# Performance work log

Measured on AMD Instinct MI355X. Metric: run time of the kernel, lower is better.

Reference implementation:

```python
import jax, jax.numpy as jnp
import numpy as np
from jax import lax

N = 8192          # river-network nodes
B = 2             # batch
T = 1024          # time steps (hours)
W = 64            # max_delay (IRF support)
H = 256           # MLP hidden dim
DT = 1.0 / 24.0   # dt in days
D_LEVELS = 8      # tree depth (4-ary tree with 8192 nodes -> depths 0..7)
BRANCH = 4


def _tree():
    parent = np.zeros(N, np.int32)
    depth = np.zeros(N, np.int32)
    for i in range(1, N):
        p = (i - 1) // BRANCH
        parent[i] = p
        depth[i] = depth[p] + 1
    parent[0] = N  # root drains to dummy sink (row N is dropped after scatter)
    return parent, depth


def setup_inputs() -> dict:
    key = jax.random.key(0)
    ks = jax.random.split(key, 6)
    parent, depth = _tree()
    return {
        "x": jax.random.uniform(ks[0], (B, N, T), dtype=jnp.float32),
        "phys": jax.random.normal(ks[1], (N, 3), dtype=jnp.float32),
        "w1": jax.random.normal(ks[2], (3, H), dtype=jnp.float32) * 0.3,
        "b1": jnp.zeros((H,), jnp.float32),
        "w2": jax.random.normal(ks[3], (H, H), dtype=jnp.float32) * 0.05,
        "b2": jnp.zeros((H,), jnp.float32),
        "w3": jax.random.normal(ks[4], (H, 2), dtype=jnp.float32) * 0.05,
        "b3": jnp.zeros((2,), jnp.float32),
        "parent": jnp.asarray(parent),
        "depth": jnp.asarray(depth),
    }


def _mlp(phys, w1, b1, w2, b2, w3, b3):
    h = jax.nn.relu(phys @ w1 + b1)
    h = jax.nn.relu(h @ w2 + b2)
    return h @ w3 + b3  # [N, 2]


def _params(phys, w1, b1, w2, b2, w3, b3):
    raw = _mlp(phys, w1, b1, w2, b2, w3, b3)
    pre_sig_off = jnp.array([0.0, 3.0], jnp.float32)
    rng = jnp.array([0.25, 1.2], jnp.float32)
    off = jnp.array([0.005, 0.0], jnp.float32)
    p = jax.nn.sigmoid(raw - pre_sig_off) * rng + off
    return p[:, 0], p[:, 1]  # Muskingum k (days), x (weight)


def _muskingum_irf(k, xw):
    # Linear-channel Muskingum IRF: pure delay k*x then exponential store k*(1-x).
    t = jnp.arange(W, dtype=jnp.float32) * DT            # [W]
    delay = (k * xw)[:, None]                            # [N, 1]
    tau = jnp.maximum(k * (1.0 - xw), 0.5 * DT)[:, None]  # keep store positive
    h = jnp.where(t[None, :] >= delay,
                  jnp.exp(-(t[None, :] - delay) / tau) / tau, 0.0)
    return h / (h.sum(-1, keepdims=True) + 1e-8)          # [N, W], unit mass


def _causal_conv(sig, irf):
    # sig [B, N, T], irf [N, W]; depthwise causal conv along time per node.
    rhs = irf[:, None, ::-1]  # [N, 1, W], reversed so correlation == convolution
    return lax.conv_general_dilated(
        sig, rhs, window_strides=(1,), padding=[(W - 1, 0)],
        dimension_numbers=("NCH", "OIH", "NCH"), feature_group_count=N)


def _route(x, irf, parent, depth):
    # Leaves-to-root routing: out[i] = irf_i * (x[i] + sum_children out[child]).
    out = jnp.zeros_like(x)
    acc = x
    for d in range(D_LEVELS - 1, -1, -1):
        mask = (depth == d)[None, :, None]
        routed = _causal_conv(acc, irf)
        contrib = jnp.where(mask, routed, 0.0)
        out = out + contrib
        upd = jnp.zeros((B, N + 1, T), x.dtype).at[:, parent, :].add(contrib)
        acc = acc + upd[:, :N, :]
    return out


def reference(x, phys, w1, b1, w2, b2, w3, b3, parent, depth):
    k, xw = _params(phys, w1, b1, w2, b2, w3, b3)
    irf = _muskingum_irf(k, xw)
    return _route(x, irf, parent, depth)  # [B, N, T]
```

## Files before the change

### kernel.cpp

```cpp
#include <hip/hip_runtime.h>
#include <hip/hip_bf16.h>

#define NN 8192
#define TT 1024
#define WW 64
#define HH 256
#define DTF (1.0f/24.0f)

typedef __attribute__((ext_vector_type(8))) short short8_t;
typedef __attribute__((ext_vector_type(4))) short short4_t;
typedef __attribute__((ext_vector_type(4))) float f32x4_t;

__device__ __forceinline__ float sigmoidf_(float v) { return 1.0f / (1.0f + __expf(-v)); }

__device__ __forceinline__ short f2bf(float f) {
    __hip_bfloat16 h = __float2bfloat16(f);
    short s; __builtin_memcpy(&s, &h, sizeof(short));
    return s;
}

__device__ __forceinline__ int swz(int e) { return e ^ (((e >> 6) & 3) << 3); }

__global__ __launch_bounds__(256) void mlp_mfma(
    const float* __restrict__ phys,
    const float* __restrict__ w1, const float* __restrict__ b1,
    const float* __restrict__ w2, const float* __restrict__ b2,
    const float* __restrict__ w3, const float* __restrict__ b3,
    float* __restrict__ irf, short* __restrict__ irfB)
{
    const int t    = threadIdx.x;
    const int wv   = t >> 6;
    const int lane = t & 63;
    const int lc = lane & 15, lg = lane >> 4;
    const int n0 = blockIdx.x * 16;

    __shared__ float s_phys[16 * 3];
    __shared__ __align__(16) short s_h1b[16 * 256];
    __shared__ float s_red[4][16][2];
    __shared__ float s_kxw[16][2];
    __shared__ __align__(16) float s_irf[16 * 64];

    if (t < 48) s_phys[t] = phys[n0 * 3 + t];
    __syncthreads();

    {
        const int m  = t >> 4;
        const int i0 = (t & 15) * 16;
        const float p0 = s_phys[m*3+0], p1 = s_phys[m*3+1], p2 = s_phys[m*3+2];
        float h[16];
#pragma unroll
        for (int u = 0; u < 4; ++u) {
            const float4 a0 = *(const float4*)&w1[0*HH + i0 + 4*u];
            const float4 a1 = *(const float4*)&w1[1*HH + i0 + 4*u];
            const float4 a2 = *(const float4*)&w1[2*HH + i0 + 4*u];
            const float4 bb = *(const float4*)&b1[i0 + 4*u];
            h[4*u+0] = fmaxf(p0*a0.x + p1*a1.x + p2*a2.x + bb.x, 0.f);
            h[4*u+1] = fmaxf(p0*a0.y + p1*a1.y + p2*a2.y + bb.y, 0.f);
            h[4*u+2] = fmaxf(p0*a0.z + p1*a1.z + p2*a2.z + bb.z, 0.f);
            h[4*u+3] = fmaxf(p0*a0.w + p1*a1.w + p2*a2.w + bb.w, 0.f);
        }
#pragma unroll
        for (int u = 0; u < 2; ++u) {
            short8_t s;
#pragma unroll
            for (int j = 0; j < 8; ++j) s[j] = f2bf(h[8*u + j]);
            *(short8_t*)&s_h1b[m * 256 + ((i0 + 8*u) ^ ((m & 7) << 3))] = s;
        }
    }
    __syncthreads();

    f32x4_t acc[4];
#pragma unroll
    for (int u = 0; u < 4; ++u) acc[u] = f32x4_t{0.f, 0.f, 0.f, 0.f};
    short8_t af[8];
#pragma unroll
    for (int ks = 0; ks < 8; ++ks)
        af[ks] = *(const short8_t*)&s_h1b[lc * 256 + ((ks*32 + 8*lg) ^ ((lc & 7) << 3))];
#pragma unroll
    for (int u = 0; u < 4; ++u) {
        const int nt = 4 * wv + u;
#pragma unroll
        for (int ks = 0; ks < 8; ++ks) {
            short8_t bfr;
#pragma unroll
            for (int j = 0; j < 8; ++j)
                bfr[j] = f2bf(w2[(ks*32 + 8*lg + j) * HH + nt*16 + lc]);
            acc[u] = __builtin_amdgcn_mfma_f32_16x16x32_bf16(af[ks], bfr, acc[u], 0, 0, 0);
        }
    }

    float p3[4][2];
#pragma unroll
    for (int q = 0; q < 4; ++q) { p3[q][0] = 0.f; p3[q][1] = 0.f; }
#pragma unroll
    for (int u = 0; u < 4; ++u) {
        const int j = (4*wv + u) * 16 + lc;
        const float b2v = b2[j];
        const float w30 = w3[j*2+0], w31 = w3[j*2+1];
#pragma unroll
        for (int q = 0; q < 4; ++q) {
            const float h2 = fmaxf(acc[u][q] + b2v, 0.f);
            p3[q][0] += h2 * w30; p3[q][1] += h2 * w31;
        }
    }
#pragma unroll
    for (int off = 8; off >= 1; off >>= 1)
#pragma unroll
        for (int q = 0; q < 4; ++q) {
            p3[q][0] += __shfl_xor(p3[q][0], off);
            p3[q][1] += __shfl_xor(p3[q][1], off);
        }
    if (lc == 0)
#pragma unroll
        for (int q = 0; q < 4; ++q) {
            s_red[wv][4*lg + q][0] = p3[q][0];
            s_red[wv][4*lg + q][1] = p3[q][1];
        }
    __syncthreads();

    if (t < 32) {
        const int m = t >> 1, d = t & 1;
        const float raw = s_red[0][m][d] + s_red[1][m][d] + s_red[2][m][d] + s_red[3][m][d] + b3[d];
        s_kxw[m][d] = (d == 0) ? sigmoidf_(raw) * 0.25f + 0.005f
                               : sigmoidf_(raw - 3.f) * 1.2f;
    }
    __syncthreads();

    {
        const int nd = t >> 4, l = t & 15;
        const float k = s_kxw[nd][0], xw = s_kxw[nd][1];
        const float delay = k * xw;
        const float tau   = fmaxf(k * (1.f - xw), 0.5f * DTF);
        float hv[4]; float s = 0.f;
#pragma unroll
        for (int u = 0; u < 4; ++u) {
            const float tf = (l + 16*u) * DTF;
            hv[u] = (tf >= delay) ? __expf(-(tf - delay) / tau) / tau : 0.f;
            s += hv[u];
        }
#pragma unroll
        for (int off = 8; off >= 1; off >>= 1) s += __shfl_xor(s, off);
        const float inv = 1.f / (s + 1e-8f);
        float* drow = irf + (size_t)(n0 + nd) * WW;
#pragma unroll
        for (int u = 0; u < 4; ++u) {
            const float v = hv[u] * inv;
            drow[l + 16*u]        = v;
            s_irf[nd*64 + l + 16*u] = v;
        }
    }
    __syncthreads();

    {
        const int nd = t >> 4, lb = t & 15;
        const float* sr = &s_irf[nd * 64];
        short* dst = irfB + (size_t)(n0 + nd) * 1536;
#pragma unroll
        for (int li = 0; li < 4; ++li) {
            const int L = 4*lb + li;
            const int Llc = L & 15, Llg = L >> 4;
#pragma unroll
            for (int p = 0; p < 3; ++p) {
                short8_t v;
#pragma unroll
                for (int j = 0; j < 8; ++j) {
                    const int idx = Llc - 8*Llg - j + 16 + 32*p;
                    v[j] = f2bf((idx >= 0 && idx < 64) ? sr[idx & 63] : 0.f);
                }
                *(short8_t*)&dst[(size_t)(p*64 + L) * 8] = v;
            }
        }
    }
}

#define LROW 1152

__device__ __forceinline__ void zero_prologue(short* sab, int tid) {
    if (tid < 10) {
        short8_t z = {0,0,0,0,0,0,0,0};
        *(short8_t*)&sab[swz(8 * tid)] = z;
    }
}

__device__ __forceinline__ void load16(const float* __restrict__ src, int tid, float (&a)[16]) {
#pragma unroll
    for (int u = 0; u < 4; ++u) {
        const float4 v = *(const float4*)&src[16 * tid + 4 * u];
        a[4*u+0] = v.x; a[4*u+1] = v.y; a[4*u+2] = v.z; a[4*u+3] = v.w;
    }
}

__device__ __forceinline__ void stage16(short* sab, const float (&a)[16], int tid) {
#pragma unroll
    for (int u = 0; u < 2; ++u) {
        short8_t s;
#pragma unroll
        for (int j = 0; j < 8; ++j) s[j] = f2bf(a[8*u + j]);
        *(short8_t*)&sab[swz(80 + 16 * tid + 8 * u)] = s;
    }
}

__device__ __forceinline__ void load_bfrags(const short* __restrict__ irfB, int n,
                                            int tid, short8_t (&bf)[3]) {
#pragma unroll
    for (int p = 0; p < 3; ++p)
        bf[p] = *(const short8_t*)&irfB[(size_t)n * 1536 + (size_t)(p*64 + tid) * 8];
}

__device__ __forceinline__ void conv_mfma3(const short* sab, const short8_t (&bf)[3],
                                           int EB, f32x4_t (&acc)[4]) {
#pragma unroll
    for (int S = 0; S < 4; ++S) {
#pragma unroll
        for (int p = 0; p < 3; ++p) {
            const short8_t af = *(const short8_t*)&sab[swz(EB + 256 * S - 16 * (2 * p + 1))];
            acc[S] = __builtin_amdgcn_mfma_f32_16x16x32_bf16(bf[p], af, acc[S], 0, 0, 0);
        }
    }
}

__global__ __launch_bounds__(256) void route_lf6p(
    const float* __restrict__ x, const short* __restrict__ irfB,
    float* __restrict__ out)
{
    const int wid = threadIdx.x >> 6;
    const int tid = threadIdx.x & 63;
    const int r   = blockIdx.x * 4 + wid;
    if (r >= 3074) return;

    const int lc = tid & 15, lg = tid >> 4;
    const int EB = 80 + 16 * lc + 8 * lg;
    const int DP = 16 * lc + 4 * lg;

    __shared__ __align__(16) short s_a[4][LROW];
    short* sab = s_a[wid];
    zero_prologue(sab, tid);

    float a16[16];
    short8_t bf[3];

    if (r < 3072) {
        const bool isl6 = (r < 1366);
        const int idx = isl6 ? r : (r - 1366);
        const int b = idx & 1;
        const int n = __builtin_amdgcn_readfirstlane((isl6 ? 1365 : 512) + (idx >> 1));
        const size_t rowb = ((size_t)b * NN + n) * TT;
        const int c0 = 4 * n + 1;

        f32x4_t accD[4];
#pragma unroll
        for (int S = 0; S < 4; ++S)
            accD[S] = *(const f32x4_t*)&x[rowb + 256 * S + DP];

#pragma unroll 1
        for (int e = 0; e < 4; ++e) {
            const int c = c0 + e;
            if (c < NN) {
                const size_t crow = ((size_t)b * NN + c) * TT;
                load16(x + crow, tid, a16);
                stage16(sab, a16, tid);
                load_bfrags(irfB, c, tid, bf);
                f32x4_t accT[4];
#pragma unroll
                for (int S = 0; S < 4; ++S) accT[S] = f32x4_t{0.f, 0.f, 0.f, 0.f};
                conv_mfma3(sab, bf, EB, accT);
#pragma unroll
                for (int S = 0; S < 4; ++S) {
                    *(f32x4_t*)&out[crow + 256 * S + DP] = accT[S];
                    accD[S] += accT[S];
                }
            }
        }

#pragma unroll
        for (int S = 0; S < 4; ++S) {
            short4_t s4;
#pragma unroll
            for (int q = 0; q < 4; ++q) s4[q] = f2bf(accD[S][q]);
            *(short4_t*)&sab[swz(80 + 256 * S + DP)] = s4;
        }

        load_bfrags(irfB, n, tid, bf);
        f32x4_t accF[4];
#pragma unroll
        for (int S = 0; S < 4; ++S) accF[S] = f32x4_t{0.f, 0.f, 0.f, 0.f};
        conv_mfma3(sab, bf, EB, accF);
#pragma unroll
        for (int S = 0; S < 4; ++S)
            *(f32x4_t*)&out[rowb + 256 * S + DP] = accF[S];
    } else {
        const int b = r - 3072;
        const int n = 2048;
        const size_t rowb = ((size_t)b * NN + n) * TT;

        load16(x + rowb, tid, a16);
        stage16(sab, a16, tid);
        load_bfrags(irfB, n, tid, bf);
        f32x4_t accF[4];
#pragma unroll
        for (int S = 0; S < 4; ++S) accF[S] = f32x4_t{0.f, 0.f, 0.f, 0.f};
        conv_mfma3(sab, bf, EB, accF);
#pragma unroll
        for (int S = 0; S < 4; ++S)
            *(f32x4_t*)&out[rowb + 256 * S + DP] = accF[S];
    }
}

__global__ __launch_bounds__(256) void route_mid_mfma(
    const float* __restrict__ x, const short* __restrict__ irfB,
    float* __restrict__ out, int base, int n_tasks)
{
    const int wid = threadIdx.x >> 6;
    const int tid = threadIdx.x & 63;
    const int r   = blockIdx.x * 4 + wid;
    if (r >= n_tasks) return;

    const int lc = tid & 15, lg = tid >> 4;
    const int EB = 80 + 16 * lc + 8 * lg;
    const int DP = 16 * lc + 4 * lg;

    __shared__ __align__(16) short s_a[4][LROW];
    short* sab = s_a[wid];
    zero_prologue(sab, tid);

    const int b = r & 1;
    const int n = __builtin_amdgcn_readfirstlane(base + (r >> 1));
    const size_t rowb = ((size_t)b * NN + n) * TT;
    const int c0 = 4 * n + 1;

    float a16[16];
#pragma unroll
    for (int u = 0; u < 4; ++u) {
        float4 v = *(const float4*)&x[rowb + 16 * tid + 4 * u];
#pragma unroll
        for (int e = 0; e < 4; ++e) {
            const float4 w = *(const float4*)&out[((size_t)b * NN + c0 + e) * TT + 16 * tid + 4 * u];
            v.x += w.x; v.y += w.y; v.z += w.z; v.w += w.w;
        }
        a16[4*u+0] = v.x; a16[4*u+1] = v.y; a16[4*u+2] = v.z; a16[4*u+3] = v.w;
    }
    stage16(sab, a16, tid);

    short8_t bf[3];
    load_bfrags(irfB, n, tid, bf);
    f32x4_t accF[4];
#pragma unroll
    for (int S = 0; S < 4; ++S) accF[S] = f32x4_t{0.f, 0.f, 0.f, 0.f};
    conv_mfma3(sab, bf, EB, accF);
#pragma unroll
    for (int S = 0; S < 4; ++S)
        *(f32x4_t*)&out[rowb + 256 * S + DP] = accF[S];
}

__global__ __launch_bounds__(256) void route_tail3_mfma(
    const float* __restrict__ x, const short* __restrict__ irfB,
    float* __restrict__ out)
{
    const int wid = threadIdx.x >> 6;
    const int tid = threadIdx.x & 63;
    const int b   = blockIdx.x & 1;
    const int p   = 5 + (int)(blockIdx.x >> 1);

    const int lc = tid & 15, lg = tid >> 4;
    const int EB = 80 + 16 * lc + 8 * lg;
    const int DP = 16 * lc + 4 * lg;

    __shared__ __align__(16) short s_a[4][LROW];
    __shared__ __align__(16) float s_ch[4][TT];
    short* sab = s_a[wid];
    zero_prologue(sab, tid);

    const int cw = 4 * p + 1 + wid;
    const size_t crow = ((size_t)b * NN + cw) * TT;

    float a16[16];
    short8_t bf[3];

    f32x4_t accCW[4];
#pragma unroll
    for (int S = 0; S < 4; ++S)
        accCW[S] = *(const f32x4_t*)&x[crow + 256 * S + DP];

#pragma unroll 1
    for (int k = 0; k < 4; ++k) {
        const int g = 4 * cw + 1 + k;
        const size_t grow = ((size_t)b * NN + g) * TT;
#pragma unroll
        for (int u = 0; u < 4; ++u) {
            float4 v = *(const float4*)&x[grow + 16 * tid + 4 * u];
#pragma unroll
            for (int e = 0; e < 4; ++e) {
                const float4 w = *(const float4*)&out[((size_t)b * NN + (4 * g + 1 + e)) * TT + 16 * tid + 4 * u];
                v.x += w.x; v.y += w.y; v.z += w.z; v.w += w.w;
            }
            a16[4*u+0] = v.x; a16[4*u+1] = v.y; a16[4*u+2] = v.z; a16[4*u+3] = v.w;
        }
        stage16(sab, a16, tid);
        load_bfrags(irfB, g, tid, bf);
        f32x4_t accT[4];
#pragma unroll
        for (int S = 0; S < 4; ++S) accT[S] = f32x4_t{0.f, 0.f, 0.f, 0.f};
        conv_mfma3(sab, bf, EB, accT);
#pragma unroll
        for (int S = 0; S < 4; ++S) {
            *(f32x4_t*)&out[grow + 256 * S + DP] = accT[S];
            accCW[S] += accT[S];
        }
    }

#pragma unroll
    for (int S = 0; S < 4; ++S) {
        short4_t s4;
#pragma unroll
        for (int q = 0; q < 4; ++q) s4[q] = f2bf(accCW[S][q]);
        *(short4_t*)&sab[swz(80 + 256 * S + DP)] = s4;
    }
    load_bfrags(irfB, cw, tid, bf);
    f32x4_t accB[4];
#pragma unroll
    for (int S = 0; S < 4; ++S) accB[S] = f32x4_t{0.f, 0.f, 0.f, 0.f};
    conv_mfma3(sab, bf, EB, accB);
#pragma unroll
    for (int S = 0; S < 4; ++S) {
        *(f32x4_t*)&out[crow + 256 * S + DP] = accB[S];
        *(f32x4_t*)&s_ch[wid][256 * S + DP]  = accB[S];
    }

    __syncthreads();

    if (wid == 0) {
        const size_t prow = ((size_t)b * NN + p) * TT;
#pragma unroll
        for (int u = 0; u < 4; ++u) {
            float4 v = *(const float4*)&x[prow + 16 * tid + 4 * u];
#pragma unroll
            for (int w2 = 0; w2 < 4; ++w2) {
                const float4 cc = *(const float4*)&s_ch[w2][16 * tid + 4 * u];
                v.x += cc.x; v.y += cc.y; v.z += cc.z; v.w += cc.w;
            }
            a16[4*u+0] = v.x; a16[4*u+1] = v.y; a16[4*u+2] = v.z; a16[4*u+3] = v.w;
        }
        stage16(sab, a16, tid);
        load_bfrags(irfB, p, tid, bf);
        f32x4_t accF[4];
#pragma unroll
        for (int S = 0; S < 4; ++S) accF[S] = f32x4_t{0.f, 0.f, 0.f, 0.f};
        conv_mfma3(sab, bf, EB, accF);
#pragma unroll
        for (int S = 0; S < 4; ++S)
            *(f32x4_t*)&out[prow + 256 * S + DP] = accF[S];
    }
}

__device__ __forceinline__ void load_rf(const float* __restrict__ irf, int n, float (&rf)[WW]) {
    const float* irp = irf + (size_t)n * WW;
#pragma unroll
    for (int i = 0; i < WW / 4; ++i) {
        const float4 f = *(const float4*)&irp[4 * i];
        rf[4*i+0] = f.x; rf[4*i+1] = f.y; rf[4*i+2] = f.z; rf[4*i+3] = f.w;
    }
}

__device__ __forceinline__ void wave_conv16(const float (&a)[16], const float (&rf)[WW],
                                            float (&y)[16], int tid)
{
#pragma unroll
    for (int j = 0; j < 16; ++j) y[j] = 0.0f;
#pragma unroll
    for (int m = 0; m < 16; ++m)
#pragma unroll
        for (int j = m; j < 16; ++j)
            y[j] += rf[j - m] * a[m];
#pragma unroll
    for (int d = 1; d <= 4; ++d) {
        float h[16];
#pragma unroll
        for (int m = 0; m < 16; ++m) {
            const float ha = __shfl(a[m], tid - d);
            h[m] = (tid >= d) ? ha : 0.0f;
        }
        if (d < 4) {
#pragma unroll
            for (int m = 0; m < 16; ++m)
#pragma unroll
                for (int j = 0; j < 16; ++j)
                    y[j] += rf[j + 16 * d - m] * h[m];
        } else {
#pragma unroll
            for (int m = 1; m < 16; ++m)
#pragma unroll
                for (int j = 0; j < m; ++j)
                    y[j] += rf[j + WW - m] * h[m];
        }
    }
}

__global__ __launch_bounds__(256) void route_tail2(
    const float* __restrict__ x, const float* __restrict__ irf,
    float* __restrict__ out)
{
    const int wid = threadIdx.x >> 6;
    const int tid = threadIdx.x & 63;
    const int b   = blockIdx.x;

    __shared__ __align__(16) float s_ch[4][TT];

    const int cw = 1 + wid;
    const size_t crow = ((size_t)b * NN + cw) * TT;
    const int loc = tid * 16;

    float rf[WW], a[16], y[16];

#pragma unroll
    for (int u = 0; u < 4; ++u) {
        float4 v = *(const float4*)&x[crow + loc + 4 * u];
#pragma unroll
        for (int e = 0; e < 4; ++e) {
            const float4 w = *(const float4*)&out[((size_t)b * NN + (4 * cw + 1 + e)) * TT + loc + 4 * u];
            v.x += w.x; v.y += w.y; v.z += w.z; v.w += w.w;
        }
        a[4*u+0] = v.x; a[4*u+1] = v.y; a[4*u+2] = v.z; a[4*u+3] = v.w;
    }
    load_rf(irf, cw, rf);
    wave_conv16(a, rf, y, tid);
#pragma unroll
    for (int u = 0; u < 4; ++u) {
        const float4 f = make_float4(y[4*u+0], y[4*u+1], y[4*u+2], y[4*u+3]);
        *(float4*)&out[crow + loc + 4 * u] = f;
        *(float4*)&s_ch[wid][loc + 4 * u]  = f;
    }

    __syncthreads();

    if (wid == 0) {
        const size_t prow = (size_t)b * NN * TT;
#pragma unroll
        for (int u = 0; u < 4; ++u) {
            float4 v = *(const float4*)&x[prow + loc + 4 * u];
#pragma unroll
            for (int w2 = 0; w2 < 4; ++w2) {
                const float4 cc = *(const float4*)&s_ch[w2][loc + 4 * u];
                v.x += cc.x; v.y += cc.y; v.z += cc.z; v.w += cc.w;
            }
            a[4*u+0] = v.x; a[4*u+1] = v.y; a[4*u+2] = v.z; a[4*u+3] = v.w;
        }
        load_rf(irf, 0, rf);
        wave_conv16(a, rf, y, tid);
#pragma unroll
        for (int u = 0; u < 4; ++u)
            *(float4*)&out[prow + loc + 4 * u] = make_float4(y[4*u+0], y[4*u+1], y[4*u+2], y[4*u+3]);
    }
}

extern "C" void kernel_launch(void* const* d_in, const int* in_sizes, int n_in,
                              void* d_out, int out_size, void* d_ws, size_t ws_size,
                              hipStream_t stream) {
    const float* x    = (const float*)d_in[0];
    const float* phys = (const float*)d_in[1];
    const float* w1   = (const float*)d_in[2];
    const float* b1   = (const float*)d_in[3];
    const float* w2   = (const float*)d_in[4];
    const float* b2   = (const float*)d_in[5];
    const float* w3   = (const float*)d_in[6];
    const float* b3   = (const float*)d_in[7];

    float* out = (float*)d_out;
    float* irf  = (float*)d_ws;
    short* irfB = (short*)((char*)d_ws + (4u << 20));

    mlp_mfma<<<512, 256, 0, stream>>>(phys, w1, b1, w2, b2, w3, b3, irf, irfB);

    route_lf6p<<<(3074 + 3) / 4, 256, 0, stream>>>(x, irfB, out);
    route_mid_mfma<<<(342 + 3) / 4, 256, 0, stream>>>(x, irfB, out, 341, 342);
    route_tail3_mfma<<<32, 256, 0, stream>>>(x, irfB, out);
    route_tail2<<<2, 256, 0, stream>>>(x, irf, out);
}
```

Measured before the change: 77.95 us.

## Fuse mid-level routing into tail kernel using 1024-thread blocks

Removes the separate route_mid_mfma launch and folds its level into the tail kernel. Each block now runs 16 waves: each wave handles one level-4 node, computing its level-5 children (or reading already-computed children when they come from the earlier kernel). Shared memory then reduces to level-3 and level-2 nodes. This saves one kernel launch and a global round trip, at the cost of 32 large blocks doing serial work with low occupancy.

Result: slower. 101.2 us (+29.8%).

```diff
diff --git a/kernel.cpp b/kernel.cpp
--- a/kernel.cpp
+++ b/kernel.cpp
@@ -306,53 +306,7 @@
     }
 }
 
-__global__ __launch_bounds__(256) void route_mid_mfma(
-    const float* __restrict__ x, const short* __restrict__ irfB,
-    float* __restrict__ out, int base, int n_tasks)
-{
-    const int wid = threadIdx.x >> 6;
-    const int tid = threadIdx.x & 63;
-    const int r   = blockIdx.x * 4 + wid;
-    if (r >= n_tasks) return;
-
-    const int lc = tid & 15, lg = tid >> 4;
-    const int EB = 80 + 16 * lc + 8 * lg;
-    const int DP = 16 * lc + 4 * lg;
-
-    __shared__ __align__(16) short s_a[4][LROW];
-    short* sab = s_a[wid];
-    zero_prologue(sab, tid);
-
-    const int b = r & 1;
-    const int n = __builtin_amdgcn_readfirstlane(base + (r >> 1));
-    const size_t rowb = ((size_t)b * NN + n) * TT;
-    const int c0 = 4 * n + 1;
-
-    float a16[16];
-#pragma unroll
-    for (int u = 0; u < 4; ++u) {
-        float4 v = *(const float4*)&x[rowb + 16 * tid + 4 * u];
-#pragma unroll
-        for (int e = 0; e < 4; ++e) {
-            const float4 w = *(const float4*)&out[((size_t)b * NN + c0 + e) * TT + 16 * tid + 4 * u];
-            v.x += w.x; v.y += w.y; v.z += w.z; v.w += w.w;
-        }
-        a16[4*u+0] = v.x; a16[4*u+1] = v.y; a16[4*u+2] = v.z; a16[4*u+3] = v.w;
-    }
-    stage16(sab, a16, tid);
-
-    short8_t bf[3];
-    load_bfrags(irfB, n, tid, bf);
-    f32x4_t accF[4];
-#pragma unroll
-    for (int S = 0; S < 4; ++S) accF[S] = f32x4_t{0.f, 0.f, 0.f, 0.f};
-    conv_mfma3(sab, bf, EB, accF);
-#pragma unroll
-    for (int S = 0; S < 4; ++S)
-        *(f32x4_t*)&out[rowb + 256 * S + DP] = accF[S];
-}
-
-__global__ __launch_bounds__(256) void route_tail3_mfma(
+__global__ __launch_bounds__(1024) void route_megatail(
     const float* __restrict__ x, const short* __restrict__ irfB,
     float* __restrict__ out)
 {
@@ -365,46 +319,54 @@
     const int EB = 80 + 16 * lc + 8 * lg;
     const int DP = 16 * lc + 4 * lg;
 
-    __shared__ __align__(16) short s_a[4][LROW];
+    __shared__ __align__(16) short s_a[16][LROW];
+    __shared__ __align__(16) float s_l4[16][TT];
     __shared__ __align__(16) float s_ch[4][TT];
     short* sab = s_a[wid];
     zero_prologue(sab, tid);
 
-    const int cw = 4 * p + 1 + wid;
-    const size_t crow = ((size_t)b * NN + cw) * TT;
+    const int g = 85 + 16 * (p - 5) + wid;
+    const size_t grow = ((size_t)b * NN + g) * TT;
 
     float a16[16];
     short8_t bf[3];
 
-    f32x4_t accCW[4];
+    f32x4_t accG[4];
 #pragma unroll
     for (int S = 0; S < 4; ++S)
-        accCW[S] = *(const f32x4_t*)&x[crow + 256 * S + DP];
+        accG[S] = *(const f32x4_t*)&x[grow + 256 * S + DP];
 
 #pragma unroll 1
     for (int k = 0; k < 4; ++k) {
-        const int g = 4 * cw + 1 + k;
-        const size_t grow = ((size_t)b * NN + g) * TT;
-#pragma unroll
-        for (int u = 0; u < 4; ++u) {
-            float4 v = *(const float4*)&x[grow + 16 * tid + 4 * u];
-#pragma unroll
-            for (int e = 0; e < 4; ++e) {
-                const float4 w = *(const float4*)&out[((size_t)b * NN + (4 * g + 1 + e)) * TT + 16 * tid + 4 * u];
-                v.x += w.x; v.y += w.y; v.z += w.z; v.w += w.w;
+        const int c5 = 4 * g + 1 + k;
+        const size_t c5row = ((size_t)b * NN + c5) * TT;
+        if (c5 < 512) {
+            const int cc0 = 4 * c5 + 1;
+#pragma unroll
+            for (int u = 0; u < 4; ++u) {
+                float4 v = *(const float4*)&x[c5row + 16 * tid + 4 * u];
+#pragma unroll
+                for (int e = 0; e < 4; ++e) {
+                    const float4 w = *(const float4*)&out[((size_t)b * NN + cc0 + e) * TT + 16 * tid + 4 * u];
+                    v.x += w.x; v.y += w.y; v.z += w.z; v.w += w.w;
+                }
+                a16[4*u+0] = v.x; a16[4*u+1] = v.y; a16[4*u+2] = v.z; a16[4*u+3] = v.w;
             }
-            a16[4*u+0] = v.x; a16[4*u+1] = v.y; a16[4*u+2] = v.z; a16[4*u+3] = v.w;
-        }
-        stage16(sab, a16, tid);
-        load_bfrags(irfB, g, tid, bf);
-        f32x4_t accT[4];
-#pragma unroll
-        for (int S = 0; S < 4; ++S) accT[S] = f32x4_t{0.f, 0.f, 0.f, 0.f};
-        conv_mfma3(sab, bf, EB, accT);
-#pragma unroll
-        for (int S = 0; S < 4; ++S) {
-            *(f32x4_t*)&out[grow + 256 * S + DP] = accT[S];
-            accCW[S] += accT[S];
+            stage16(sab, a16, tid);
+            load_bfrags(irfB, c5, tid, bf);
+            f32x4_t accT[4];
+#pragma unroll
+            for (int S = 0; S < 4; ++S) accT[S] = f32x4_t{0.f, 0.f, 0.f, 0.f};
+            conv_mfma3(sab, bf, EB, accT);
+#pragma unroll
+            for (int S = 0; S < 4; ++S) {
+                *(f32x4_t*)&out[c5row + 256 * S + DP] = accT[S];
+                accG[S] += accT[S];
+            }
+        } else {
+#pragma unroll
+            for (int S = 0; S < 4; ++S)
+                accG[S] += *(const f32x4_t*)&out[c5row + 256 * S + DP];
         }
     }
 
@@ -412,35 +374,71 @@
     for (int S = 0; S < 4; ++S) {
         short4_t s4;
 #pragma unroll
-        for (int q = 0; q < 4; ++q) s4[q] = f2bf(accCW[S][q]);
+        for (int q = 0; q < 4; ++q) s4[q] = f2bf(accG[S][q]);
         *(short4_t*)&sab[swz(80 + 256 * S + DP)] = s4;
     }
-    load_bfrags(irfB, cw, tid, bf);
-    f32x4_t accB[4];
-#pragma unroll
-    for (int S = 0; S < 4; ++S) accB[S] = f32x4_t{0.f, 0.f, 0.f, 0.f};
-    conv_mfma3(sab, bf, EB, accB);
+    load_bfrags(irfB, g, tid, bf);
+    f32x4_t accL4[4];
+#pragma unroll
+    for (int S = 0; S < 4; ++S) accL4[S] = f32x4_t{0.f, 0.f, 0.f, 0.f};
+    conv_mfma3(sab, bf, EB, accL4);
 #pragma unroll
     for (int S = 0; S < 4; ++S) {
-        *(f32x4_t*)&out[crow + 256 * S + DP] = accB[S];
-        *(f32x4_t*)&s_ch[wid][256 * S + DP]  = accB[S];
+        *(f32x4_t*)&out[grow + 256 * S + DP] = accL4[S];
+        *(f32x4_t*)&s_l4[wid][256 * S + DP]  = accL4[S];
+    }
+
+    __syncthreads();
+
+    if (wid < 4) {
+        const int cw = 21 + 4 * (p - 5) + wid;
+        const size_t crow = ((size_t)b * NN + cw) * TT;
+        f32x4_t accC[4];
+#pragma unroll
+        for (int S = 0; S < 4; ++S) {
+            accC[S] = *(const f32x4_t*)&x[crow + 256 * S + DP];
+#pragma unroll
+            for (int k = 0; k < 4; ++k)
+                accC[S] += *(const f32x4_t*)&s_l4[4 * wid + k][256 * S + DP];
+        }
+#pragma unroll
+        for (int S = 0; S < 4; ++S) {
+            short4_t s4;
+#pragma unroll
+            for (int q = 0; q < 4; ++q) s4[q] = f2bf(accC[S][q]);
+            *(short4_t*)&sab[swz(80 + 256 * S + DP)] = s4;
+        }
+        load_bfrags(irfB, cw, tid, bf);
+        f32x4_t accB[4];
+#pragma unroll
+        for (int S = 0; S < 4; ++S) accB[S] = f32x4_t{0.f, 0.f, 0.f, 0.f};
+        conv_mfma3(sab, bf, EB, accB);
+#pragma unroll
+        for (int S = 0; S < 4; ++S) {
+            *(f32x4_t*)&out[crow + 256 * S + DP] = accB[S];
+            *(f32x4_t*)&s_ch[wid][256 * S + DP]  = accB[S];
+        }
     }
 
     __syncthreads();
 
     if (wid == 0) {
         const size_t prow = ((size_t)b * NN + p) * TT;
-#pragma unroll
-        for (int u = 0; u < 4; ++u) {
-            float4 v = *(const float4*)&x[prow + 16 * tid + 4 * u];
-#pragma unroll
-            for (int w2 = 0; w2 < 4; ++w2) {
-                const float4 cc = *(const float4*)&s_ch[w2][16 * tid + 4 * u];
-                v.x += cc.x; v.y += cc.y; v.z += cc.z; v.w += cc.w;
-            }
-            a16[4*u+0] = v.x; a16[4*u+1] = v.y; a16[4*u+2] = v.z; a16[4*u+3] = v.w;
-        }
-        stage16(sab, a16, tid);
+        f32x4_t accP[4];
+#pragma unroll
+        for (int S = 0; S < 4; ++S) {
+            accP[S] = *(const f32x4_t*)&x[prow + 256 * S + DP];
+#pragma unroll
+            for (int k = 0; k < 4; ++k)
+                accP[S] += *(const f32x4_t*)&s_ch[k][256 * S + DP];
+        }
+#pragma unroll
+        for (int S = 0; S < 4; ++S) {
+            short4_t s4;
+#pragma unroll
+            for (int q = 0; q < 4; ++q) s4[q] = f2bf(accP[S][q]);
+            *(short4_t*)&sab[swz(80 + 256 * S + DP)] = s4;
+        }
         load_bfrags(irfB, p, tid, bf);
         f32x4_t accF[4];
 #pragma unroll
@@ -571,7 +569,6 @@
     mlp_mfma<<<512, 256, 0, stream>>>(phys, w1, b1, w2, b2, w3, b3, irf, irfB);
 
     route_lf6p<<<(3074 + 3) / 4, 256, 0, stream>>>(x, irfB, out);
-    route_mid_mfma<<<(342 + 3) / 4, 256, 0, stream>>>(x, irfB, out, 341, 342);
-    route_tail3_mfma<<<32, 256, 0, stream>>>(x, irfB, out);
+    route_megatail<<<32, 1024, 0, stream>>>(x, irfB, out);
     route_tail2<<<2, 256, 0, stream>>>(x, irf, out);
 }
```
